# Optimization experiments

Hardware: AMD Instinct MI355X
Metric: run time of the kernel (lower is better)

The kernel has to match this reference:

```python
import jax, jax.numpy as jnp
import numpy as np

C = 64  # num_channels
B, H, W = 16, 160, 160


def squeeze2d(x, f=2):
    b, c, h, w = x.shape
    x = x.reshape(b, c, h // f, f, w // f, f)
    x = x.transpose(0, 1, 3, 5, 2, 4)
    return x.reshape(b, c * f * f, h // f, w // f)


def unsqueeze2d(x, f=2):
    b, c, h, w = x.shape
    x = x.reshape(b, c // (f * f), f, f, h, w)
    x = x.transpose(0, 1, 4, 2, 5, 3)
    return x.reshape(b, c // (f * f), h * f, w * f)


def get_indices(num_channels):
    # generate_ind(p) tiles the row-major-flattened 2x2 pattern over C//4 channel groups
    def gen(p):
        return np.tile(np.array(p, dtype=bool), num_channels // 4)
    m = np.ones(num_channels, dtype=bool)
    t = gen([0, 0, 1, 1]); b = ~t
    l = gen([0, 1, 0, 1]); r = ~l
    return (m, t, b, l, r, t & l, t & r, b & l, b & r)


INDS = get_indices(C)


def conv1x1(z, w):
    # 1x1 conv == channel matmul
    return jnp.einsum('oc,bchw->bohw', w, z)


def partition_input(x):
    z = unsqueeze2d(x)
    z = jnp.pad(z, ((0, 0), (0, 0), (1, 1), (1, 1)), constant_values=-1.0)
    z = squeeze2d(z)  # (B, C, H+1, W+1)
    m, t, b, l, r, tl, tr, bl, br = INDS
    return (z[:, :, 1:-1, 1:-1],
            z[:, t, :1, 1:-1], z[:, b, -1:, 1:-1],
            z[:, l, 1:-1, :1], z[:, r, 1:-1, -1:],
            z[:, tl, :1, :1], z[:, tr, :1, -1:],
            z[:, bl, -1:, :1], z[:, br, -1:, -1:])


def unsqueeze_line(ze):
    b, c = ze.shape[:2]
    sz = (1, -1) if ze.shape[-2] == 1 else (-1, 1)
    return ze.reshape(b, c // 2, 2, -1).transpose(0, 1, 3, 2).reshape(b, c // 2, *sz)


def merge_output(z_m, z_t, z_b, z_l, z_r, z_tl, z_tr, z_bl, z_br):
    z_m = unsqueeze2d(z_m)
    z_t, z_b, z_l, z_r = [unsqueeze_line(zi) for zi in (z_t, z_b, z_l, z_r)]
    z_tt = jnp.concatenate([z_tl, z_t, z_tr], axis=3)
    z_mm = jnp.concatenate([z_l, z_m, z_r], axis=3)
    z_bb = jnp.concatenate([z_bl, z_b, z_br], axis=3)
    return squeeze2d(jnp.concatenate([z_tt, z_mm, z_bb], axis=2))


def setup_inputs() -> dict:
    key = jax.random.key(0)
    k1, k2 = jax.random.split(key)
    x = jax.random.normal(k1, (B, C, H, W), dtype=jnp.float32)
    logdet = jax.random.normal(k2, (B,), dtype=jnp.float32)
    rng = np.random.RandomState(0)
    w_init = np.linalg.qr(rng.randn(C, C))[0].astype(np.float32)
    weight = jnp.asarray(w_init)
    return {"input": x, "logdet": logdet, "weight": weight}


def reference(input, logdet, weight):
    h, w = input.shape[-2:]
    pixels = [(h - 1) * (w - 1), w - 1, w - 1, h - 1, h - 1, 1, 1, 1, 1]
    ws = [weight[np.ix_(ind, ind)] for ind in INDS]
    dlogdet = sum(jnp.linalg.slogdet(wi)[1] * p for wi, p in zip(ws, pixels))
    zs = partition_input(input)
    outs = [conv1x1(z, wi) for z, wi in zip(zs, ws)]
    output = merge_output(*outs)
    return output, logdet + dlogdet
```

## Files before the change

### kernel.cpp

```cpp
#include <hip/hip_runtime.h>
#include <math.h>

#define NB 16
#define NC 64
#define HW 160
#define PLANE (HW * HW)
#define SG 161
#define SGSQ (SG * SG)
#define NSITES (NB * SGSQ)
#define OUT_LD_OFF (NB * NC * PLANE)
#define TILE 256
#define NCONV ((NSITES + TILE - 1) / TILE)

#define SMEM_FLOATS 5320

__device__ inline int chmap(int i, int n, int pa, int pb) {
    if (n == 64) return i;
    if (n == 32) return ((i >> 1) << 2) | ((i & 1) ? pb : pa);
    return (i << 2) | pa;
}

template <int N>
__device__ float group_lu_logabsdet(const float* __restrict__ W, float* A,
                                    int pa, int pb, int lane) {
    const int r = lane & (N - 1);
    constexpr int LD = N + 1;
#pragma unroll 4
    for (int i = 0; i < N; ++i)
        A[i * LD + r] = W[chmap(i, N, pa, pb) * 64 + chmap(r, N, pa, pb)];
    asm volatile("s_waitcnt lgkmcnt(0) vmcnt(0)" ::: "memory");
    float logdet = 0.f;
    for (int k = 0; k < N; ++k) {
        float cand = (r >= k) ? fabsf(A[r * LD + k]) : -1.f;
        int idx = r;
#pragma unroll
        for (int off = N >> 1; off; off >>= 1) {
            float oc = __shfl_xor(cand, off, N);
            int oi = __shfl_xor(idx, off, N);
            if (oc > cand || (oc == cand && oi < idx)) { cand = oc; idx = oi; }
        }
        const int p = idx;
        if (p != k) {
            float tk = A[k * LD + r];
            float tp = A[p * LD + r];
            A[k * LD + r] = tp;
            A[p * LD + r] = tk;
        }
        asm volatile("s_waitcnt lgkmcnt(0)" ::: "memory");
        float piv = A[k * LD + k];
        logdet += logf(fabsf(piv));
        float rpiv = 1.f / piv;
        if (r > k) {
            float wk = A[k * LD + r] * rpiv;
            int i = k + 1;
            for (; i + 3 < N; i += 4) {
                float a0 = A[(i + 0) * LD + k], a1 = A[(i + 1) * LD + k],
                      a2 = A[(i + 2) * LD + k], a3 = A[(i + 3) * LD + k];
                float x0 = A[(i + 0) * LD + r], x1 = A[(i + 1) * LD + r],
                      x2 = A[(i + 2) * LD + r], x3 = A[(i + 3) * LD + r];
                A[(i + 0) * LD + r] = fmaf(-a0, wk, x0);
                A[(i + 1) * LD + r] = fmaf(-a1, wk, x1);
                A[(i + 2) * LD + r] = fmaf(-a2, wk, x2);
                A[(i + 3) * LD + r] = fmaf(-a3, wk, x3);
            }
            for (; i < N; ++i) {
                float a0 = A[i * LD + k], x0 = A[i * LD + r];
                A[i * LD + r] = fmaf(-a0, wk, x0);
            }
        }
        asm volatile("s_waitcnt lgkmcnt(0)" ::: "memory");
    }
    return logdet;
}

#define LOADCH(dst, cc)                                                      \
    {                                                                        \
        _Pragma("unroll") for (int i = 0; i < 16; ++i)                       \
            dst[i] = xb[(size_t)(((cc) << 4) + (i ^ 3)) * PLANE +            \
                        aoff[i & 3]];                                        \
    }

#define COMPCH(src, cc)                                                      \
    {                                                                        \
        _Pragma("unroll") for (int i = 0; i < 16; ++i) src[i] *= mf[i & 3];  \
        _Pragma("unroll") for (int j = 0; j < 32; ++j) {                     \
            const float* wr = wbase + j * 64 + ((cc) << 4);                  \
            float4 w0 = *(const float4*)(wr + 0);                            \
            float4 w1 = *(const float4*)(wr + 4);                            \
            float4 w2 = *(const float4*)(wr + 8);                            \
            float4 w3 = *(const float4*)(wr + 12);                           \
            float a = u[j];                                                  \
            a = fmaf(w0.x, src[0], a);  a = fmaf(w0.y, src[1], a);           \
            a = fmaf(w0.z, src[2], a);  a = fmaf(w0.w, src[3], a);           \
            a = fmaf(w1.x, src[4], a);  a = fmaf(w1.y, src[5], a);           \
            a = fmaf(w1.z, src[6], a);  a = fmaf(w1.w, src[7], a);           \
            a = fmaf(w2.x, src[8], a);  a = fmaf(w2.y, src[9], a);           \
            a = fmaf(w2.z, src[10], a); a = fmaf(w2.w, src[11], a);          \
            a = fmaf(w3.x, src[12], a); a = fmaf(w3.y, src[13], a);          \
            a = fmaf(w3.z, src[14], a); a = fmaf(w3.w, src[15], a);          \
            u[j] = a;                                                        \
        }                                                                    \
    }

__global__ __launch_bounds__(256, 5) void InvConv1x1GridAlign_kernel(
    const float* __restrict__ x, const float* __restrict__ ld_in,
    const float* __restrict__ W, float* __restrict__ out) {
    __shared__ __align__(16) float smem[SMEM_FLOATS];
    const int tid = threadIdx.x;

    if (blockIdx.x == 0) {
        float* A = smem;
        float* partial = smem + 5312;
        float* pivslot = smem + 5316;
        const int lane = tid & 63;
        const int wid = tid >> 6;
        for (int e = tid; e < 64 * 64; e += 256)
            A[(e >> 6) * 65 + (e & 63)] = W[e];
        __syncthreads();
        float logdet64 = 0.f;
        for (int k = 0; k < 64; ++k) {
            if (wid == 0) {
                float cand = (lane >= k) ? fabsf(A[lane * 65 + k]) : -1.f;
                int idx = lane;
#pragma unroll
                for (int off = 32; off; off >>= 1) {
                    float oc = __shfl_xor(cand, off, 64);
                    int oi = __shfl_xor(idx, off, 64);
                    if (oc > cand || (oc == cand && oi < idx)) {
                        cand = oc;
                        idx = oi;
                    }
                }
                const int p = idx;
                if (p != k) {
                    float tk = A[k * 65 + lane];
                    float tp = A[p * 65 + lane];
                    A[k * 65 + lane] = tp;
                    A[p * 65 + lane] = tk;
                }
                asm volatile("s_waitcnt lgkmcnt(0)" ::: "memory");
                if (lane == 0) pivslot[0] = A[k * 65 + k];
            }
            __syncthreads();
            const float piv = pivslot[0];
            logdet64 += logf(fabsf(piv));
            const float rpiv = 1.f / piv;
            const float akr = A[k * 65 + lane];
            int i = k + 1 + wid;
            for (; i + 12 < 64; i += 16) {
                float a0 = A[(i + 0) * 65 + k], a1 = A[(i + 4) * 65 + k],
                      a2 = A[(i + 8) * 65 + k], a3 = A[(i + 12) * 65 + k];
                float x0 = A[(i + 0) * 65 + lane], x1 = A[(i + 4) * 65 + lane],
                      x2 = A[(i + 8) * 65 + lane], x3 = A[(i + 12) * 65 + lane];
                A[(i + 0) * 65 + lane] = fmaf(-(a0 * rpiv), akr, x0);
                A[(i + 4) * 65 + lane] = fmaf(-(a1 * rpiv), akr, x1);
                A[(i + 8) * 65 + lane] = fmaf(-(a2 * rpiv), akr, x2);
                A[(i + 12) * 65 + lane] = fmaf(-(a3 * rpiv), akr, x3);
            }
            for (; i < 64; i += 4) {
                float a0 = A[i * 65 + k];
                A[i * 65 + lane] = fmaf(-(a0 * rpiv), akr, A[i * 65 + lane]);
            }
            asm volatile("s_waitcnt lgkmcnt(0)" ::: "memory");
            __syncthreads();
        }
        if (tid == 0) partial[0] = 25281.f * logdet64;
        __syncthreads();
        if (wid == 1) {
            int g = lane >> 5;
            float ld = group_lu_logabsdet<32>(W, A + g * 1056, g ? 0 : 2,
                                              g ? 1 : 3, lane);
            float part = (__shfl(ld, 0, 64) + __shfl(ld, 32, 64)) * 159.f;
            if (lane == 0) partial[1] = part;
        } else if (wid == 2) {
            int g = lane >> 5;
            float ld = group_lu_logabsdet<32>(W, A + 2112 + g * 1056,
                                              g ? 0 : 1, g ? 2 : 3, lane);
            float part = (__shfl(ld, 0, 64) + __shfl(ld, 32, 64)) * 159.f;
            if (lane == 0) partial[2] = part;
        } else if (wid == 3) {
            int g = lane >> 4;
            float ld = group_lu_logabsdet<16>(W, A + 4224 + g * 272, 3 - g, 0,
                                              lane);
            float part = __shfl(ld, 0, 64) + __shfl(ld, 16, 64) +
                         __shfl(ld, 32, 64) + __shfl(ld, 48, 64);
            if (lane == 0) partial[3] = part;
        }
        __syncthreads();
        if (tid < NB) {
            float dl = partial[0] + partial[1] + partial[2] + partial[3];
            out[OUT_LD_OFF + tid] = ld_in[tid] + dl;
        }
        return;
    }

    const int cbid = (int)blockIdx.x - 1;
    const int ohalf = cbid & 1;
    const int s = (cbid >> 1) * TILE + tid;

    const int offm[4] = {0, 1, HW, HW + 1};
    bool vm[4];
    int aoff[4];
    float mf[4];
    int baseoff;
    const float* xb;
    float* ob;
    {
        bool sok = s < NSITES;
        unsigned us = (unsigned)(sok ? s : 0);
        unsigned b = us / SGSQ;
        unsigned rr = us - b * SGSQ;
        unsigned Y = rr / SG;
        unsigned X = rr - Y * SG;
        xb = x + (size_t)b * (NC * PLANE);
        ob = out + (size_t)b * (NC * PLANE);
        baseoff = ((int)Y - 1) * HW + ((int)X - 1);
        bool okT = sok && (Y >= 1), okB = sok && (Y <= HW - 1);
        bool okL = (X >= 1), okR = (X <= HW - 1);
        vm[0] = okT && okL; vm[1] = okT && okR;
        vm[2] = okB && okL; vm[3] = okB && okR;
#pragma unroll
        for (int m = 0; m < 4; ++m) {
            aoff[m] = vm[m] ? (baseoff + offm[m]) : 0;
            mf[m] = vm[m] ? 1.f : 0.f;
        }
    }

    const float* wbase = W + (ohalf << 5) * 64;

    float u[32];
#pragma unroll
    for (int j = 0; j < 32; ++j) u[j] = 0.f;

    float va[16], vb[16];
    LOADCH(va, 0)
    LOADCH(vb, 1)
    COMPCH(va, 0)
    LOADCH(va, 2)
    COMPCH(vb, 1)
    LOADCH(vb, 3)
    COMPCH(va, 2)
    COMPCH(vb, 3)

#pragma unroll
    for (int m = 0; m < 4; ++m) {
        if (vm[m]) {
#pragma unroll
            for (int t = 0; t < 8; ++t) {
                int j = (t << 2) + m;
                ob[(size_t)((ohalf << 5) + (j ^ 3)) * PLANE + baseoff +
                   offm[m]] = u[j];
            }
        }
    }
}

extern "C" void kernel_launch(void* const* d_in, const int* in_sizes, int n_in,
                              void* d_out, int out_size, void* d_ws, size_t ws_size,
                              hipStream_t stream) {
    const float* x = (const float*)d_in[0];
    const float* ld = (const float*)d_in[1];
    const float* W = (const float*)d_in[2];
    float* out = (float*)d_out;
    hipLaunchKernelGGL(InvConv1x1GridAlign_kernel, dim3(2 * NCONV + 1),
                       dim3(256), 0, stream, x, ld, W, out);
}
```

Before: 257.9 us.

## Compute all 64 output channels per thread instead of splitting into halves

Each thread now accumulates all 64 output channels for its site, which halves the grid and means every input value is loaded from global memory once instead of twice. The channel-group loop becomes a non-unrolled loop of two iterations that keeps the double-buffered loads. In exchange the accumulator doubles to 64 registers and launch bounds drop from 5 to 4 waves per SIMD, which lowers occupancy and the ability to hide memory latency.

```diff
diff --git a/kernel.cpp b/kernel.cpp
--- a/kernel.cpp
+++ b/kernel.cpp
@@ -76,15 +76,15 @@
 #define LOADCH(dst, cc)                                                      \
     {                                                                        \
         _Pragma("unroll") for (int i = 0; i < 16; ++i)                       \
-            dst[i] = xb[(size_t)(((cc) << 4) + (i ^ 3)) * PLANE +            \
+            dst[i] = xb[(size_t)((((cc) << 4) + (i ^ 3)) * PLANE) +          \
                         aoff[i & 3]];                                        \
     }
 
 #define COMPCH(src, cc)                                                      \
     {                                                                        \
         _Pragma("unroll") for (int i = 0; i < 16; ++i) src[i] *= mf[i & 3];  \
-        _Pragma("unroll") for (int j = 0; j < 32; ++j) {                     \
-            const float* wr = wbase + j * 64 + ((cc) << 4);                  \
+        _Pragma("unroll") for (int j = 0; j < 64; ++j) {                     \
+            const float* wr = W + j * 64 + ((cc) << 4);                      \
             float4 w0 = *(const float4*)(wr + 0);                            \
             float4 w1 = *(const float4*)(wr + 4);                            \
             float4 w2 = *(const float4*)(wr + 8);                            \
@@ -102,7 +102,7 @@
         }                                                                    \
     }
 
-__global__ __launch_bounds__(256, 5) void InvConv1x1GridAlign_kernel(
+__global__ __launch_bounds__(256, 4) void InvConv1x1GridAlign_kernel(
     const float* __restrict__ x, const float* __restrict__ ld_in,
     const float* __restrict__ W, float* __restrict__ out) {
     __shared__ __align__(16) float smem[SMEM_FLOATS];
@@ -194,9 +194,7 @@
         return;
     }
 
-    const int cbid = (int)blockIdx.x - 1;
-    const int ohalf = cbid & 1;
-    const int s = (cbid >> 1) * TILE + tid;
+    const int s = ((int)blockIdx.x - 1) * TILE + tid;
 
     const int offm[4] = {0, 1, HW, HW + 1};
     bool vm[4];
@@ -226,30 +224,27 @@
         }
     }
 
-    const float* wbase = W + (ohalf << 5) * 64;
-
-    float u[32];
-#pragma unroll
-    for (int j = 0; j < 32; ++j) u[j] = 0.f;
+    float u[64];
+#pragma unroll
+    for (int j = 0; j < 64; ++j) u[j] = 0.f;
 
     float va[16], vb[16];
     LOADCH(va, 0)
-    LOADCH(vb, 1)
-    COMPCH(va, 0)
-    LOADCH(va, 2)
-    COMPCH(vb, 1)
-    LOADCH(vb, 3)
-    COMPCH(va, 2)
-    COMPCH(vb, 3)
+#pragma unroll 1
+    for (int cc = 0; cc < 4; cc += 2) {
+        LOADCH(vb, cc + 1)
+        COMPCH(va, cc)
+        if (cc + 2 < 4) LOADCH(va, cc + 2)
+        COMPCH(vb, cc + 1)
+    }
 
 #pragma unroll
     for (int m = 0; m < 4; ++m) {
         if (vm[m]) {
 #pragma unroll
-            for (int t = 0; t < 8; ++t) {
+            for (int t = 0; t < 16; ++t) {
                 int j = (t << 2) + m;
-                ob[(size_t)((ohalf << 5) + (j ^ 3)) * PLANE + baseoff +
-                   offm[m]] = u[j];
+                ob[(size_t)((j ^ 3) * PLANE) + baseoff + offm[m]] = u[j];
             }
         }
     }
@@ -262,6 +257,6 @@
     const float* ld = (const float*)d_in[1];
     const float* W = (const float*)d_in[2];
     float* out = (float*)d_out;
-    hipLaunchKernelGGL(InvConv1x1GridAlign_kernel, dim3(2 * NCONV + 1),
-                       dim3(256), 0, stream, x, ld, W, out);
-}
+    hipLaunchKernelGGL(InvConv1x1GridAlign_kernel, dim3(NCONV + 1), dim3(256),
+                       0, stream, x, ld, W, out);
+}
```

Measured after the change: 307.4 us. 1.19x slower.

## Replace 64x64 LU with single-wavefront blocked panel factorization

Applied to the files above, without the earlier changes.

The full 64x64 LU used for the main log-determinant now runs in one wavefront. Panels of 8 columns are kept in registers and factored with cross-lane shuffles, followed by row swaps, a triangular solve and a rank-8 trailing update in shared memory. This removes the 128 block-wide barriers per factorization that block 0 paid in the old scheme, where four wavefronts took turns. In exchange the trailing update is done by one wavefront instead of four. The cost only matters if block 0's serial determinant work is on the kernel's critical path.

```diff
diff --git a/kernel.cpp b/kernel.cpp
--- a/kernel.cpp
+++ b/kernel.cpp
@@ -111,60 +111,101 @@
     if (blockIdx.x == 0) {
         float* A = smem;
         float* partial = smem + 5312;
-        float* pivslot = smem + 5316;
         const int lane = tid & 63;
         const int wid = tid >> 6;
-        for (int e = tid; e < 64 * 64; e += 256)
-            A[(e >> 6) * 65 + (e & 63)] = W[e];
-        __syncthreads();
-        float logdet64 = 0.f;
-        for (int k = 0; k < 64; ++k) {
-            if (wid == 0) {
-                float cand = (lane >= k) ? fabsf(A[lane * 65 + k]) : -1.f;
-                int idx = lane;
-#pragma unroll
-                for (int off = 32; off; off >>= 1) {
-                    float oc = __shfl_xor(cand, off, 64);
-                    int oi = __shfl_xor(idx, off, 64);
-                    if (oc > cand || (oc == cand && oi < idx)) {
-                        cand = oc;
-                        idx = oi;
+
+        if (wid == 0) {
+            const int r = lane;
+            for (int e = lane; e < 64 * 64; e += 64)
+                A[(e >> 6) * 65 + (e & 63)] = W[e];
+            asm volatile("s_waitcnt lgkmcnt(0) vmcnt(0)" ::: "memory");
+            float ll = 0.f;
+#pragma unroll 1
+            for (int p8 = 0; p8 < 8; ++p8) {
+                const int k0 = p8 << 3;
+                float a[8];
+#pragma unroll
+                for (int c = 0; c < 8; ++c) a[c] = A[r * 65 + k0 + c];
+                int pivs[8];
+#pragma unroll
+                for (int t = 0; t < 8; ++t) {
+                    const int k = k0 + t;
+                    float cand = (r >= k) ? fabsf(a[t]) : -1.f;
+                    int idx = r;
+#pragma unroll
+                    for (int off = 32; off; off >>= 1) {
+                        float oc = __shfl_xor(cand, off, 64);
+                        int oi = __shfl_xor(idx, off, 64);
+                        if (oc > cand || (oc == cand && oi < idx)) {
+                            cand = oc;
+                            idx = oi;
+                        }
+                    }
+                    const int prow = idx;
+                    float apk = __shfl(a[t], prow, 64);
+                    ll += logf(fabsf(apk));
+                    float rpiv = 1.f / apk;
+                    pivs[t] = prow;
+#pragma unroll
+                    for (int c = 0; c < 8; ++c) {
+                        float vk = __shfl(a[c], k, 64);
+                        float vp = __shfl(a[c], prow, 64);
+                        a[c] = (r == k) ? vp : ((r == prow) ? vk : a[c]);
+                    }
+                    if (r > k) a[t] *= rpiv;
+#pragma unroll
+                    for (int c = t + 1; c < 8; ++c) {
+                        float ukc = __shfl(a[c], k, 64);
+                        if (r > k) a[c] = fmaf(-a[t], ukc, a[c]);
                     }
                 }
-                const int p = idx;
-                if (p != k) {
-                    float tk = A[k * 65 + lane];
-                    float tp = A[p * 65 + lane];
-                    A[k * 65 + lane] = tp;
-                    A[p * 65 + lane] = tk;
+#pragma unroll
+                for (int c = 0; c < 8; ++c) A[r * 65 + k0 + c] = a[c];
+                asm volatile("s_waitcnt lgkmcnt(0)" ::: "memory");
+                const int ncols = 64 - k0 - 8;
+                if (ncols > 0) {
+                    const int j = k0 + 8 + r;
+                    const bool jok = r < ncols;
+#pragma unroll
+                    for (int t = 0; t < 8; ++t) {
+                        const int k = k0 + t, p_ = pivs[t];
+                        if (p_ != k && jok) {
+                            float hk = A[k * 65 + j];
+                            float hp = A[p_ * 65 + j];
+                            A[k * 65 + j] = hp;
+                            A[p_ * 65 + j] = hk;
+                        }
+                    }
+                    float u[8];
+#pragma unroll
+                    for (int t = 0; t < 8; ++t)
+                        u[t] = jok ? A[(k0 + t) * 65 + j] : 0.f;
+#pragma unroll
+                    for (int t = 1; t < 8; ++t)
+#pragma unroll
+                        for (int s2 = 0; s2 < t; ++s2) {
+                            float lts = A[(k0 + t) * 65 + k0 + s2];
+                            u[t] = fmaf(-lts, u[s2], u[t]);
+                        }
+                    if (jok) {
+#pragma unroll
+                        for (int t = 1; t < 8; ++t) A[(k0 + t) * 65 + j] = u[t];
+                    }
+#pragma unroll 4
+                    for (int i = k0 + 8; i < 64; ++i) {
+                        float acc2 = jok ? A[i * 65 + j] : 0.f;
+#pragma unroll
+                        for (int t = 0; t < 8; ++t) {
+                            float lit = A[i * 65 + k0 + t];
+                            acc2 = fmaf(-lit, u[t], acc2);
+                        }
+                        if (jok) A[i * 65 + j] = acc2;
+                    }
+                    asm volatile("s_waitcnt lgkmcnt(0)" ::: "memory");
                 }
-                asm volatile("s_waitcnt lgkmcnt(0)" ::: "memory");
-                if (lane == 0) pivslot[0] = A[k * 65 + k];
             }
-            __syncthreads();
-            const float piv = pivslot[0];
-            logdet64 += logf(fabsf(piv));
-            const float rpiv = 1.f / piv;
-            const float akr = A[k * 65 + lane];
-            int i = k + 1 + wid;
-            for (; i + 12 < 64; i += 16) {
-                float a0 = A[(i + 0) * 65 + k], a1 = A[(i + 4) * 65 + k],
-                      a2 = A[(i + 8) * 65 + k], a3 = A[(i + 12) * 65 + k];
-                float x0 = A[(i + 0) * 65 + lane], x1 = A[(i + 4) * 65 + lane],
-                      x2 = A[(i + 8) * 65 + lane], x3 = A[(i + 12) * 65 + lane];
-                A[(i + 0) * 65 + lane] = fmaf(-(a0 * rpiv), akr, x0);
-                A[(i + 4) * 65 + lane] = fmaf(-(a1 * rpiv), akr, x1);
-                A[(i + 8) * 65 + lane] = fmaf(-(a2 * rpiv), akr, x2);
-                A[(i + 12) * 65 + lane] = fmaf(-(a3 * rpiv), akr, x3);
-            }
-            for (; i < 64; i += 4) {
-                float a0 = A[i * 65 + k];
-                A[i * 65 + lane] = fmaf(-(a0 * rpiv), akr, A[i * 65 + lane]);
-            }
-            asm volatile("s_waitcnt lgkmcnt(0)" ::: "memory");
-            __syncthreads();
-        }
-        if (tid == 0) partial[0] = 25281.f * logdet64;
+            if (lane == 0) partial[0] = 25281.f * ll;
+        }
         __syncthreads();
         if (wid == 1) {
             int g = lane >> 5;
```

New measurement: 240.8 us. 6.6% less time.
